# Kernel tuning notes

Hardware: AMD Instinct MI355X
Metric: run time of the kernel (lower is better)

The kernel has to match this reference:

```python
import jax, jax.numpy as jnp
import numpy as np

N = 120000   # current nodes
F = 256      # num_feat
H = 256      # num_hidden
L = 64       # num_logits
E_MP = 1000000  # message-passing edges
E = 200000      # scored edges
PREV = [60000, 80000, 100000]
PROX_WEIGHT = 0.3


def setup_inputs() -> dict:
    key = jax.random.key(0)
    ks = jax.random.split(key, 40)
    n = lambda k, shape, s=0.05: jax.random.normal(k, shape, dtype=jnp.float32) * s
    inp = {}
    inp["x"] = n(ks[0], (N, F), 1.0)
    inp["mp_adj"] = jax.random.randint(ks[1], (2, E_MP), 0, N)
    inp["edges"] = jax.random.randint(ks[2], (2, E), 0, N)
    inp["index"] = jax.random.randint(ks[3], (E,), 0, E)
    inp["prev_emb0"] = n(ks[4], (PREV[0], H), 1.0)
    inp["prev_emb1"] = n(ks[5], (PREV[1], H), 1.0)
    inp["prev_emb2"] = n(ks[6], (PREV[2], H), 1.0)
    # Module_L params
    inp["gc1_W"] = n(ks[7], (F, H))
    inp["gc1_b"] = jnp.zeros((H,), jnp.float32)
    inp["gc2_W"] = n(ks[8], (H, H))
    inp["gc2_b"] = jnp.zeros((H,), jnp.float32)
    inp["linear_W"] = n(ks[9], (2 * H, H))
    inp["linear_b"] = jnp.zeros((H,), jnp.float32)
    inp["weight_lin"] = n(ks[10], (H, H))
    inp["bias_lin"] = jnp.zeros((H,), jnp.float32)
    inp["w_q"] = n(ks[11], (H, H))
    inp["w_k"] = n(ks[12], (H, H))
    inp["w_v"] = n(ks[13], (H, H))
    # ensemble params
    inp["ml_w1"] = n(ks[14], (2 * H, H)); inp["ml_b1"] = jnp.zeros((H,), jnp.float32)
    inp["ml_w2"] = n(ks[15], (H, 1));     inp["ml_b2"] = jnp.zeros((1,), jnp.float32)
    inp["ms_w1"] = n(ks[16], (2 * H, H)); inp["ms_b1"] = jnp.zeros((H,), jnp.float32)
    inp["ms_w2"] = n(ks[17], (H, 1));     inp["ms_b2"] = jnp.zeros((1,), jnp.float32)
    inp["msdr_w"] = n(ks[18], (L, H));    inp["msdr_b"] = jnp.zeros((H,), jnp.float32)
    # Module_S logits and precomputed score tables
    inp["logits"] = n(ks[19], (N, L), 1.0)
    inp["ms_train_score"] = jax.random.uniform(ks[20], (E,), dtype=jnp.float32)
    inp["prox_train_score"] = jax.random.uniform(ks[21], (E,), dtype=jnp.float32)
    return inp


def _gcn(x, W, b, src, dst, n_nodes):
    xw = x @ W
    loop = jnp.arange(n_nodes)
    s = jnp.concatenate([src, loop])
    d = jnp.concatenate([dst, loop])
    deg = jax.ops.segment_sum(jnp.ones_like(d, dtype=xw.dtype), d, num_segments=n_nodes)
    dinv = jax.lax.rsqrt(jnp.maximum(deg, 1.0))
    norm = (dinv[s] * dinv[d])[:, None]
    out = jax.ops.segment_sum(xw[s] * norm, d, num_segments=n_nodes)
    return out + b


def _mean_max(a, b):
    return jnp.concatenate([(a + b) * 0.5, jnp.maximum(a, b)], axis=1)


def reference(x, mp_adj, edges, index, prev_emb0, prev_emb1, prev_emb2,
              gc1_W, gc1_b, gc2_W, gc2_b, linear_W, linear_b,
              weight_lin, bias_lin, w_q, w_k, w_v,
              ml_w1, ml_b1, ml_w2, ml_b2, ms_w1, ms_b1, ms_w2, ms_b2,
              msdr_w, msdr_b, logits, ms_train_score, prox_train_score):
    src_mp, dst_mp = mp_adj[0], mp_adj[1]
    # --- Module_L: 2-layer GCN encoder (dropout = identity in eval) ---
    h = jnp.tanh(_gcn(x, gc1_W, gc1_b, src_mp, dst_mp, N))
    emb = jnp.tanh(_gcn(h, gc2_W, gc2_b, src_mp, dst_mp, N))

    # --- ragged per-window temporal attention over previous snapshots ---
    prev = [prev_emb0, prev_emb1, prev_emb2]
    T = len(prev)
    start = 0
    parts = []
    for i in range(T):
        end = prev[i].shape[0]
        if end == N:
            break
        # stack snapshots i..T-1 plus current, restricted to window [start:end)
        stack = jnp.stack([prev[j][start:end] for j in range(i, T)] + [emb[start:end]], axis=0)  # [S,n,H]
        q = emb[start:end] @ w_q              # [n,H]
        k = stack @ w_k                        # [S,n,H]
        v = stack @ w_v                        # [S,n,H]
        attn = jnp.einsum('nh,snh->ns', q, k) / np.sqrt(np.float32(H))
        w = jax.nn.softmax(attn, axis=-1)      # [n,S]
        parts.append(jnp.einsum('ns,snh->nh', w, v))
        start = end
    if start != N:
        parts.append(emb[start:] @ w_v)
    attn_emb = jnp.concatenate(parts, axis=0)  # [N,H]

    emb2 = jnp.tanh(jnp.concatenate([emb, attn_emb], axis=1) @ linear_W + linear_b)  # [N,H]

    # --- symmetric bilinear edge scores ---
    sym = (weight_lin + weight_lin.T) * 0.5
    es, ed = edges[0], edges[1]
    sim = ((emb2[es] @ sym) * emb2[ed] + bias_lin).sum(axis=1)
    ml_scores = jax.nn.sigmoid(sim)            # [E]

    # --- Module_S / Proximity: table lookups ---
    ms_scores = ms_train_score[index]
    prox_scores = prox_train_score[index]

    # --- ensemble weighted sum ---
    scores = jnp.stack([ml_scores, ms_scores, prox_scores], axis=1)  # [E,3]
    ml_feat = _mean_max(emb2[es], emb2[ed])                          # [E,2H]
    a_ml = jnp.tanh(jnp.tanh(ml_feat @ ml_w1 + ml_b1) @ ml_w2 + ml_b2)
    r0 = jnp.tanh(logits[es] @ msdr_w + msdr_b)
    r1 = jnp.tanh(logits[ed] @ msdr_w + msdr_b)
    a_ms = jnp.tanh(jnp.tanh(_mean_max(r0, r1) @ ms_w1 + ms_b1) @ ms_w2 + ms_b2)
    a_px = jnp.full_like(a_ml, PROX_WEIGHT)
    attn_w = jax.nn.softmax(jnp.concatenate([a_ml, a_ms, a_px], axis=1), axis=1)  # [E,3]
    final = jnp.clip((scores * attn_w).sum(axis=1), 0.0, 1.0)
    return final
```

## Files before the change

kernel.cpp:

```cpp
#include <hip/hip_runtime.h>
#include <hip/hip_bf16.h>

#define Nn_   120000
#define F_    256
#define H_    256
#define L_    64
#define EMP_  1000000
#define E_    200000
#define P0_   60000
#define P1_   80000
#define P2_   100000
#define PROXW 0.3f

typedef __attribute__((ext_vector_type(8))) short bf16x8;
typedef __attribute__((ext_vector_type(4))) float f32x4;

__device__ inline float bf2f(unsigned short u) {
    union { unsigned int i; float f; } x; x.i = ((unsigned int)u) << 16; return x.f;
}
__device__ inline unsigned short f2bf(float f) {
    union { float f; unsigned int i; } x; x.f = f;
    unsigned int r = x.i + 0x7fffu + ((x.i >> 16) & 1u);
    return (unsigned short)(r >> 16);
}
__device__ inline float tanh_fast(float x) {
    float e = __expf(2.0f * x);
    return 1.0f - 2.0f * __builtin_amdgcn_rcpf(e + 1.0f);
}
__device__ inline float sigmoid_fast(float z) {
    return __builtin_amdgcn_rcpf(1.0f + __expf(-z));
}
__device__ inline int lds_off(int row, int s) {
    return row * 64 + ((s ^ ((row >> 1) & 3)) << 4);
}
__device__ inline void gload_lds16(const void* g, void* l) {
    __builtin_amdgcn_global_load_lds((const __attribute__((address_space(1))) void*)g,
                                     (__attribute__((address_space(3))) void*)l, 16, 0, 0);
}
__device__ inline void unpk8(uint4 u, float* o) {
    o[0] = bf2f(u.x & 0xffff); o[1] = bf2f(u.x >> 16);
    o[2] = bf2f(u.y & 0xffff); o[3] = bf2f(u.y >> 16);
    o[4] = bf2f(u.z & 0xffff); o[5] = bf2f(u.z >> 16);
    o[6] = bf2f(u.w & 0xffff); o[7] = bf2f(u.w >> 16);
}

__global__ void k_count(const int* __restrict__ dst, int* __restrict__ cnt, int n) {
    int e = blockIdx.x * 256 + threadIdx.x;
    if (e < n) atomicAdd(&cnt[dst[e]], 1);
}
__global__ void k_block_reduce(const int* __restrict__ cnt, int* __restrict__ bsum, int n) {
    __shared__ int s[256];
    int i = blockIdx.x * 256 + threadIdx.x;
    s[threadIdx.x] = (i < n) ? cnt[i] : 0;
    __syncthreads();
    for (int o = 128; o > 0; o >>= 1) {
        if (threadIdx.x < o) s[threadIdx.x] += s[threadIdx.x + o];
        __syncthreads();
    }
    if (threadIdx.x == 0) bsum[blockIdx.x] = s[0];
}
__global__ void k_scan_bsum(int* bsum, int nb) {
    if (threadIdx.x == 0 && blockIdx.x == 0) {
        int acc = 0;
        for (int i = 0; i < nb; i++) { int v = bsum[i]; bsum[i] = acc; acc += v; }
    }
}
__global__ void k_scan_final(const int* __restrict__ cnt, const int* __restrict__ bsum,
                             int* __restrict__ rowp, int n, int etot) {
    __shared__ int s[256];
    int tid = threadIdx.x;
    int i = blockIdx.x * 256 + tid;
    int v = (i < n) ? cnt[i] : 0;
    s[tid] = v;
    __syncthreads();
    for (int o = 1; o < 256; o <<= 1) {
        int t = 0;
        if (tid >= o) t = s[tid - o];
        __syncthreads();
        s[tid] += t;
        __syncthreads();
    }
    if (i < n) rowp[i] = bsum[blockIdx.x] + s[tid] - v;
    if (i == 0 && blockIdx.x == 0) rowp[n] = etot;
}
__global__ void k_fill(const int* __restrict__ src, const int* __restrict__ dst,
                       const int* __restrict__ rowp, int* __restrict__ fill,
                       int* __restrict__ csr, int n) {
    int e = blockIdx.x * 256 + threadIdx.x;
    if (e < n) {
        int d = dst[e];
        int p = atomicAdd(&fill[d], 1);
        csr[rowp[d] + p] = src[e];
    }
}
__global__ void k_dinv(const int* __restrict__ cnt, float* __restrict__ dinv, int n) {
    int i = blockIdx.x * 256 + threadIdx.x;
    if (i < n) dinv[i] = rsqrtf((float)cnt[i] + 1.0f);
}

#define TM 64
#define TN 64
#define TK 16
template <bool TRANSB>
__global__ void gemm_tiled(const float* __restrict__ A, const float* __restrict__ B,
                           float* __restrict__ C, int M, int K, int N) {
    __shared__ float As[TK][TM + 4];
    __shared__ float Bs[TK][TN + 4];
    int tid = threadIdx.x;
    int tx = tid & 15, ty = tid >> 4;
    int row0 = blockIdx.y * TM, col0 = blockIdx.x * TN;
    int lr = tid >> 2, lc4 = (tid & 3) * 4;
    float acc[4][4] = {};
    for (int k0 = 0; k0 < K; k0 += TK) {
        {
            int gr = row0 + lr;
            float4 v = make_float4(0.f, 0.f, 0.f, 0.f);
            if (gr < M) v = *(const float4*)(A + (size_t)gr * K + k0 + lc4);
            As[lc4 + 0][lr] = v.x; As[lc4 + 1][lr] = v.y;
            As[lc4 + 2][lr] = v.z; As[lc4 + 3][lr] = v.w;
        }
        {
            int n = tid & 63, kk0 = tid >> 6;
#pragma unroll
            for (int p = 0; p < 4; p++) {
                int kk = kk0 + p * 4;
                if (TRANSB) Bs[kk][n] = B[(size_t)(col0 + n) * K + k0 + kk];
                else        Bs[kk][n] = B[(size_t)(k0 + kk) * N + col0 + n];
            }
        }
        __syncthreads();
#pragma unroll
        for (int kk = 0; kk < TK; kk++) {
            float4 a = *(const float4*)&As[kk][ty * 4];
            float4 b = *(const float4*)&Bs[kk][tx * 4];
            float av[4] = {a.x, a.y, a.z, a.w};
            float bv[4] = {b.x, b.y, b.z, b.w};
#pragma unroll
            for (int i = 0; i < 4; i++)
#pragma unroll
                for (int j = 0; j < 4; j++) acc[i][j] += av[i] * bv[j];
        }
        __syncthreads();
    }
#pragma unroll
    for (int i = 0; i < 4; i++) {
        int r = row0 + ty * 4 + i;
        if (r >= M) continue;
#pragma unroll
        for (int j = 0; j < 4; j++) C[(size_t)r * N + col0 + tx * 4 + j] = acc[i][j];
    }
}

__global__ void k_cvt(const float* __restrict__ in, unsigned short* __restrict__ out, int n4) {
    int i = blockIdx.x * 256 + threadIdx.x;
    if (i >= n4) return;
    float4 v = ((const float4*)in)[i];
    ushort4 o;
    o.x = f2bf(v.x); o.y = f2bf(v.y); o.z = f2bf(v.z); o.w = f2bf(v.w);
    ((ushort4*)out)[i] = o;
}
__global__ void k_transpose_cvt(const float* __restrict__ W, unsigned short* __restrict__ Wt,
                                int R, int C) {
    int c = blockIdx.x;
    for (int r = threadIdx.x; r < R; r += 256)
        Wt[(size_t)c * R + r] = f2bf(W[(size_t)r * C + c]);
}
__global__ void k_sym_cvt(const float* __restrict__ W, unsigned short* __restrict__ symb) {
    int r = blockIdx.x, c = threadIdx.x;
    symb[r * 256 + c] = f2bf(0.5f * (W[r * 256 + c] + W[c * 256 + r]));
}
__global__ void k_bt512(const float* __restrict__ linW, const float* __restrict__ W2w,
                        unsigned short* __restrict__ Bt) {
    int idx = blockIdx.x * 256 + threadIdx.x;
    int n = idx >> 9, k = idx & 511;
    float v = (k < 256) ? linW[(size_t)k * 256 + n] : W2w[(size_t)(k - 256) * 256 + n];
    Bt[idx] = f2bf(v);
}
__global__ void k_sumb(const float* __restrict__ b, float* __restrict__ out) {
    __shared__ float s[256];
    int tid = threadIdx.x;
    s[tid] = b[tid];
    __syncthreads();
    for (int o = 128; o > 0; o >>= 1) {
        if (tid < o) s[tid] += s[tid + o];
        __syncthreads();
    }
    if (tid == 0) out[0] = s[0];
}
__global__ void k_packBF(const float* __restrict__ Wsrc, unsigned short* __restrict__ P) {
    int t = blockIdx.x * 256 + threadIdx.x;
    if (t >= 16384) return;
    int c = t >> 6, l = t & 63;
    int os = c >> 5, half = (c >> 4) & 1, colb = c & 15;
    int col = (colb << 4) + (l & 15);
    int k = (half << 8) + (os << 5) + ((l >> 4) << 3);
    bf16x8 v;
#pragma unroll
    for (int j = 0; j < 8; ++j) v[j] = (short)f2bf(Wsrc[(size_t)(k + j) * 256 + col]);
    *(bf16x8*)(P + (size_t)t * 8) = v;
}

__global__ __launch_bounds__(256)
void k_agg_bf(const unsigned short* __restrict__ xw, const int* __restrict__ rowp,
              const int* __restrict__ csr, const float* __restrict__ dinv,
              const float* __restrict__ bias, unsigned short* __restrict__ out) {
    int w = threadIdx.x >> 6, lane = threadIdx.x & 63;
    int v = blockIdx.x * 4 + w;
    if (v >= Nn_) return;
    const uint2* x64 = (const uint2*)xw;
    float a0 = 0.f, a1 = 0.f, a2 = 0.f, a3 = 0.f;
    int beg = rowp[v], end = rowp[v + 1];
    uint2 un = make_uint2(0, 0); float dn = 0.f;
    if (beg < end) {
        int s0 = csr[beg];
        dn = dinv[s0];
        un = x64[(size_t)s0 * 64 + lane];
    }
    for (int p = beg; p < end; ++p) {
        uint2 uc = un; float dc = dn;
        if (p + 1 < end) {
            int s1 = csr[p + 1];
            dn = dinv[s1];
            un = x64[(size_t)s1 * 64 + lane];
        }
        a0 += bf2f(uc.x & 0xffff) * dc;
        a1 += bf2f(uc.x >> 16) * dc;
        a2 += bf2f(uc.y & 0xffff) * dc;
        a3 += bf2f(uc.y >> 16) * dc;
    }
    float dv = dinv[v];
    uint2 us = x64[(size_t)v * 64 + lane];
    a0 = a0 * dv + bf2f(us.x & 0xffff) * dv * dv;
    a1 = a1 * dv + bf2f(us.x >> 16) * dv * dv;
    a2 = a2 * dv + bf2f(us.y & 0xffff) * dv * dv;
    a3 = a3 * dv + bf2f(us.y >> 16) * dv * dv;
    int c0 = lane * 4;
    float4 bv = *(const float4*)(bias + c0);
    uint2 ov;
    ov.x = (unsigned int)f2bf(tanh_fast(a0 + bv.x)) |
           ((unsigned int)f2bf(tanh_fast(a1 + bv.y)) << 16);
    ov.y = (unsigned int)f2bf(tanh_fast(a2 + bv.z)) |
           ((unsigned int)f2bf(tanh_fast(a3 + bv.w)) << 16);
    ((uint2*)out)[(size_t)v * 64 + lane] = ov;
}

template <bool BIAS, bool TANH>
__global__ __launch_bounds__(256)
void mfma_gemm(const unsigned short* __restrict__ A0, const unsigned short* __restrict__ A1,
               int Ksplit, int K, const unsigned short* __restrict__ Bt,
               const float* __restrict__ bias, unsigned short* __restrict__ Cb, int M) {
    __shared__ char lds[2][16384];
    int tid = threadIdx.x, lane = tid & 63, w = tid >> 6;
    int row0 = blockIdx.y * 128, col0 = blockIdx.x * 128;
    int wr = w >> 1, wc = w & 1;
    f32x4 acc[4][4] = {};
    int nk = K >> 5;

    auto stage = [&](int ks, int buf) {
        int k0 = ks << 5;
        #pragma unroll
        for (int j = 0; j < 4; ++j) {
            int ins = w + (j << 2);
            int lrow = ((ins & 7) << 4) + (lane >> 2);
            int p = lane & 3;
            int slog = p ^ ((lrow >> 1) & 3);
            char* ldst = lds[buf] + ((ins & 7) << 10) + ((ins >= 8) ? 8192 : 0);
            const unsigned short* src;
            if (ins < 8) {
                int grow = row0 + lrow;
                if (grow >= M) grow = M - 1;
                const unsigned short* Asrc; int kk, pitch;
                if (k0 < Ksplit) { Asrc = A0; kk = k0; pitch = Ksplit; }
                else             { Asrc = A1; kk = k0 - Ksplit; pitch = K - Ksplit; }
                src = Asrc + (size_t)grow * pitch + kk + (slog << 3);
            } else {
                int grow = col0 + lrow;
                src = Bt + (size_t)grow * K + k0 + (slog << 3);
            }
            gload_lds16(src, ldst);
        }
    };

    stage(0, 0);
    for (int ks = 0; ks < nk; ++ks) {
        int cur = ks & 1;
        if (ks + 1 < nk) {
            stage(ks + 1, cur ^ 1);
            asm volatile("s_waitcnt vmcnt(4)" ::: "memory");
        } else {
            asm volatile("s_waitcnt vmcnt(0)" ::: "memory");
        }
        __builtin_amdgcn_s_barrier();
        __builtin_amdgcn_sched_barrier(0);
        int s = lane >> 4, r16 = lane & 15;
        bf16x8 a[4], b[4];
        #pragma unroll
        for (int m = 0; m < 4; ++m) a[m] = *(const bf16x8*)(lds[cur] + lds_off(wr * 64 + m * 16 + r16, s));
        #pragma unroll
        for (int n = 0; n < 4; ++n) b[n] = *(const bf16x8*)(lds[cur] + 8192 + lds_off(wc * 64 + n * 16 + r16, s));
        __builtin_amdgcn_s_setprio(1);
        #pragma unroll
        for (int m = 0; m < 4; ++m)
            #pragma unroll
            for (int n = 0; n < 4; ++n)
                acc[m][n] = __builtin_amdgcn_mfma_f32_16x16x32_bf16(a[m], b[n], acc[m][n], 0, 0, 0);
        __builtin_amdgcn_s_setprio(0);
        __builtin_amdgcn_s_barrier();
        __builtin_amdgcn_sched_barrier(0);
    }
    int q = lane >> 4, r16 = lane & 15;
    float bv[4];
    #pragma unroll
    for (int n = 0; n < 4; ++n) bv[n] = BIAS ? bias[col0 + wc * 64 + n * 16 + r16] : 0.f;
    #pragma unroll
    for (int m = 0; m < 4; ++m) {
        #pragma unroll
        for (int i = 0; i < 4; ++i) {
            int row = row0 + wr * 64 + m * 16 + q * 4 + i;
            if (row >= M) continue;
            #pragma unroll
            for (int n = 0; n < 4; ++n) {
                int col = col0 + wc * 64 + n * 16 + r16;
                float v = acc[m][n][i];
                if (BIAS) v += bv[n];
                if (TANH) v = tanh_fast(v);
                Cb[(size_t)row * 256 + col] = f2bf(v);
            }
        }
    }
}

__global__ __launch_bounds__(256)
void k_attn_u2(const unsigned short* __restrict__ emb, const unsigned short* __restrict__ t,
               const float* __restrict__ p0, const float* __restrict__ p1,
               const float* __restrict__ p2, unsigned short* __restrict__ u) {
    int tid = threadIdx.x;
    int g = tid >> 4, l = tid & 15;
    int n = blockIdx.x * 16 + g;
    size_t eoff = (size_t)n * 256 + l * 16;
    const uint4* e16 = (const uint4*)(emb + eoff);
    uint4* u16 = (uint4*)(u + eoff);
    uint4 eb0 = e16[0], eb1 = e16[1];
    if (n >= P2_) { u16[0] = eb0; u16[1] = eb1; return; }
    float tv[16], ev[16];
    {
        const uint4* t16 = (const uint4*)(t + eoff);
        unpk8(t16[0], tv); unpk8(t16[1], tv + 8);
        unpk8(eb0, ev); unpk8(eb1, ev + 8);
    }
    float m = -3.0e38f, den = 0.f, o[16];
    #pragma unroll
    for (int i = 0; i < 16; i++) o[i] = 0.f;
    auto accum = [&](const float* sv) {
        float dt = 0.f;
        #pragma unroll
        for (int i = 0; i < 16; i++) dt += tv[i] * sv[i];
        dt += __shfl_xor(dt, 1);
        dt += __shfl_xor(dt, 2);
        dt += __shfl_xor(dt, 4);
        dt += __shfl_xor(dt, 8);
        float lg = dt * 0.0625f;
        float mn = fmaxf(m, lg);
        float s0 = __expf(m - mn), s1 = __expf(lg - mn);
        den = den * s0 + s1;
        #pragma unroll
        for (int i = 0; i < 16; i++) o[i] = o[i] * s0 + s1 * sv[i];
        m = mn;
    };
    auto accum_f32 = [&](const float* base) {
        float sv[16];
        const float4* b4 = (const float4*)(base + eoff);
        #pragma unroll
        for (int i = 0; i < 4; i++) {
            float4 q = b4[i];
            sv[4 * i] = q.x; sv[4 * i + 1] = q.y; sv[4 * i + 2] = q.z; sv[4 * i + 3] = q.w;
        }
        accum(sv);
    };
    if (n < P0_)      { accum_f32(p0); accum_f32(p1); accum_f32(p2); }
    else if (n < P1_) { accum_f32(p1); accum_f32(p2); }
    else              { accum_f32(p2); }
    accum(ev);
    float inv = __builtin_amdgcn_rcpf(den);
    unsigned short h[16];
    #pragma unroll
    for (int i = 0; i < 16; i++) h[i] = f2bf(o[i] * inv);
    uint4 r0, r1;
    r0.x = h[0] | ((unsigned int)h[1] << 16);  r0.y = h[2] | ((unsigned int)h[3] << 16);
    r0.z = h[4] | ((unsigned int)h[5] << 16);  r0.w = h[6] | ((unsigned int)h[7] << 16);
    r1.x = h[8] | ((unsigned int)h[9] << 16);  r1.y = h[10] | ((unsigned int)h[11] << 16);
    r1.z = h[12] | ((unsigned int)h[13] << 16); r1.w = h[14] | ((unsigned int)h[15] << 16);
    u16[0] = r0; u16[1] = r1;
}

template <bool SIM>
__global__ __launch_bounds__(256)
void mfma_edge3(const unsigned short* __restrict__ srcemb, const unsigned short* __restrict__ gsrc,
                const int* __restrict__ es, const int* __restrict__ ed,
                const unsigned short* __restrict__ PkF, const float* __restrict__ b1,
                const float* __restrict__ w2, const float* __restrict__ sumb,
                float* __restrict__ a_pre, float* __restrict__ mlsc) {
    __shared__ char lds[8192];
    __shared__ float red[64];
    int tid = threadIdx.x, lane = tid & 63, w = tid >> 6;
    int e0 = blockIdx.x * 64;
    int arow = tid >> 2, p = tid & 3;
    int ia = es[e0 + arow], ib = ed[e0 + arow];
    const unsigned short* ra = srcemb + (size_t)ia * 256;
    const unsigned short* rb = srcemb + (size_t)ib * 256;
    const unsigned short* rg = SIM ? (gsrc + (size_t)ia * 256) : nullptr;
    int slog = p ^ ((arow >> 1) & 3);
    int abase = arow * 64 + (p << 4);
    if (tid < 64) red[tid] = 0.f;
    float simacc = 0.f;
    f32x4 acc[4][4] = {};
    uint4 pa = *(const uint4*)(ra + (slog << 3));
    uint4 pb = *(const uint4*)(rb + (slog << 3));
    uint4 pg = make_uint4(0, 0, 0, 0);
    if (SIM) pg = *(const uint4*)(rg + (slog << 3));
    const bf16x8* BF = (const bf16x8*)PkF;
    for (int os = 0; os < 8; ++os) {
        {
            float fa[8], fb[8];
            unpk8(pa, fa); unpk8(pb, fb);
            bf16x8 vm, vx;
            #pragma unroll
            for (int i = 0; i < 8; i++) {
                vm[i] = (short)f2bf(0.5f * (fa[i] + fb[i]));
                vx[i] = (short)f2bf(fmaxf(fa[i], fb[i]));
            }
            *(bf16x8*)(lds + abase) = vm;
            *(bf16x8*)(lds + 4096 + abase) = vx;
            if (SIM) {
                float fg[8];
                unpk8(pg, fg);
                #pragma unroll
                for (int i = 0; i < 8; i++) simacc += fg[i] * fb[i];
            }
        }
        bf16x8 b0[4];
        #pragma unroll
        for (int n2 = 0; n2 < 4; ++n2)
            b0[n2] = BF[(((os << 1) << 4) + (w << 2) + n2) * 64 + lane];
        if (os < 7) {
            int cb = ((os + 1) << 5) + (slog << 3);
            pa = *(const uint4*)(ra + cb);
            pb = *(const uint4*)(rb + cb);
            if (SIM) pg = *(const uint4*)(rg + cb);
        }
        asm volatile("s_waitcnt lgkmcnt(0)" ::: "memory");
        __builtin_amdgcn_s_barrier();
        __builtin_amdgcn_sched_barrier(0);
        int s = lane >> 4, r16 = lane & 15;
        {
            bf16x8 a[4];
            #pragma unroll
            for (int m2 = 0; m2 < 4; ++m2)
                a[m2] = *(const bf16x8*)(lds + lds_off(m2 * 16 + r16, s));
            __builtin_amdgcn_s_setprio(1);
            #pragma unroll
            for (int m2 = 0; m2 < 4; ++m2)
                #pragma unroll
                for (int n2 = 0; n2 < 4; ++n2)
                    acc[m2][n2] = __builtin_amdgcn_mfma_f32_16x16x32_bf16(a[m2], b0[n2], acc[m2][n2], 0, 0, 0);
            __builtin_amdgcn_s_setprio(0);
        }
        {
            bf16x8 b1r[4], a[4];
            #pragma unroll
            for (int n2 = 0; n2 < 4; ++n2)
                b1r[n2] = BF[((((os << 1) + 1) << 4) + (w << 2) + n2) * 64 + lane];
            #pragma unroll
            for (int m2 = 0; m2 < 4; ++m2)
                a[m2] = *(const bf16x8*)(lds + 4096 + lds_off(m2 * 16 + r16, s));
            __builtin_amdgcn_s_setprio(1);
            #pragma unroll
            for (int m2 = 0; m2 < 4; ++m2)
                #pragma unroll
                for (int n2 = 0; n2 < 4; ++n2)
                    acc[m2][n2] = __builtin_amdgcn_mfma_f32_16x16x32_bf16(a[m2], b1r[n2], acc[m2][n2], 0, 0, 0);
            __builtin_amdgcn_s_setprio(0);
        }
        __builtin_amdgcn_s_barrier();
        __builtin_amdgcn_sched_barrier(0);
    }
    int q = lane >> 4, r16 = lane & 15;
    float b1c[4], w2c[4];
    #pragma unroll
    for (int n2 = 0; n2 < 4; ++n2) {
        int c = (w << 6) + n2 * 16 + r16;
        b1c[n2] = b1[c]; w2c[n2] = w2[c];
    }
    #pragma unroll
    for (int m2 = 0; m2 < 4; ++m2) {
        #pragma unroll
        for (int i = 0; i < 4; ++i) {
            int row = m2 * 16 + q * 4 + i;
            float ps = 0.f;
            #pragma unroll
            for (int n2 = 0; n2 < 4; ++n2) ps += tanh_fast(acc[m2][n2][i] + b1c[n2]) * w2c[n2];
            ps += __shfl_xor(ps, 1);
            ps += __shfl_xor(ps, 2);
            ps += __shfl_xor(ps, 4);
            ps += __shfl_xor(ps, 8);
            if (r16 == 0) atomicAdd(&red[row], ps);
        }
    }
    if (SIM) {
        simacc += __shfl_xor(simacc, 1);
        simacc += __shfl_xor(simacc, 2);
        if (p == 0) mlsc[e0 + arow] = sigmoid_fast(simacc + sumb[0]);
    }
    __syncthreads();
    if (tid < 64) a_pre[e0 + tid] = red[tid];
}

__global__ void k_final(const float* __restrict__ apml, const float* __restrict__ apms,
                        const float* __restrict__ mlsc, const float* __restrict__ mstr,
                        const float* __restrict__ pxtr, const int* __restrict__ index,
                        const float* __restrict__ mlb2, const float* __restrict__ msb2,
                        float* __restrict__ out) {
    int e = blockIdx.x * 256 + threadIdx.x;
    if (e >= E_) return;
    float aml = tanh_fast(apml[e] + mlb2[0]);
    float ams = tanh_fast(apms[e] + msb2[0]);
    float apx = PROXW;
    float m = fmaxf(aml, fmaxf(ams, apx));
    float wml = __expf(aml - m), wms = __expf(ams - m), wpx = __expf(apx - m);
    float inv = __builtin_amdgcn_rcpf(wml + wms + wpx);
    int idx = index[e];
    float v = (mlsc[e] * wml + mstr[idx] * wms + pxtr[idx] * wpx) * inv;
    out[e] = fminf(fmaxf(v, 0.f), 1.f);
}

__global__ void k_sentinel(float* out, int n) {
    int i = blockIdx.x * 256 + threadIdx.x;
    if (i < n) out[i] = -12345.0f;
}

extern "C" void kernel_launch(void* const* d_in, const int* in_sizes, int n_in,
                              void* d_out, int out_size, void* d_ws, size_t ws_size,
                              hipStream_t stream) {
    const float* x     = (const float*)d_in[0];
    const int*   mp    = (const int*)d_in[1];
    const int*   edges = (const int*)d_in[2];
    const int*   index = (const int*)d_in[3];
    const float* p0    = (const float*)d_in[4];
    const float* p1    = (const float*)d_in[5];
    const float* p2    = (const float*)d_in[6];
    const float* gc1W  = (const float*)d_in[7];
    const float* gc1b  = (const float*)d_in[8];
    const float* gc2W  = (const float*)d_in[9];
    const float* gc2b  = (const float*)d_in[10];
    const float* linW  = (const float*)d_in[11];
    const float* linb  = (const float*)d_in[12];
    const float* wlin  = (const float*)d_in[13];
    const float* blin  = (const float*)d_in[14];
    const float* wq    = (const float*)d_in[15];
    const float* wk    = (const float*)d_in[16];
    const float* wv    = (const float*)d_in[17];
    const float* mlw1  = (const float*)d_in[18];
    const float* mlb1  = (const float*)d_in[19];
    const float* mlw2  = (const float*)d_in[20];
    const float* mlb2  = (const float*)d_in[21];
    const float* msw1  = (const float*)d_in[22];
    const float* msb1  = (const float*)d_in[23];
    const float* msw2  = (const float*)d_in[24];
    const float* msb2  = (const float*)d_in[25];
    const float* msdrW = (const float*)d_in[26];
    const float* msdrb = (const float*)d_in[27];
    const float* logits = (const float*)d_in[28];
    const float* mstr  = (const float*)d_in[29];
    const float* pxtr  = (const float*)d_in[30];
    float* out = (float*)d_out;

    const int* src_mp = mp;
    const int* dst_mp = mp + EMP_;
    const int* es = edges;
    const int* ed = edges + E_;

    char* ws = (char*)d_ws;
    size_t off = 0;
    auto alloc = [&](size_t bytes) -> char* {
        off = (off + 255) & ~(size_t)255;
        char* r = ws + off;
        off += bytes;
        return r;
    };
    const size_t NODE_BF = (size_t)Nn_ * 256 * 2;
    unsigned short* W0 = (unsigned short*)alloc(NODE_BF);
    unsigned short* W1 = (unsigned short*)alloc(NODE_BF);
    unsigned short* W2 = (unsigned short*)alloc(NODE_BF);
    unsigned short* W3 = (unsigned short*)alloc(NODE_BF);
    unsigned short* W4 = (unsigned short*)alloc(NODE_BF);
    unsigned short* W5 = (unsigned short*)alloc(NODE_BF);
    int*   cnt  = (int*)alloc((size_t)Nn_ * 4);
    int*   rowp = (int*)alloc((size_t)(Nn_ + 1) * 4);
    int*   fill = (int*)alloc((size_t)Nn_ * 4);
    int*   csr  = (int*)alloc((size_t)EMP_ * 4);
    float* dinv = (float*)alloc((size_t)Nn_ * 4);
    int*   bsum = (int*)alloc(512 * 4);
    float* Mqk  = (float*)alloc(65536 * 4);
    float* W2wf = (float*)alloc(65536 * 4);
    unsigned short* gc1Wt = (unsigned short*)alloc(65536 * 2);
    unsigned short* gc2Wt = (unsigned short*)alloc(65536 * 2);
    unsigned short* MqkT  = (unsigned short*)alloc(65536 * 2);
    unsigned short* Bt512 = (unsigned short*)alloc(131072 * 2);
    unsigned short* symb  = (unsigned short*)alloc(65536 * 2);
    unsigned short* msdrWt = (unsigned short*)alloc(16384 * 2);
    unsigned short* mlPk  = (unsigned short*)alloc(131072 * 2);
    unsigned short* msPk  = (unsigned short*)alloc(131072 * 2);
    float* apml = (float*)alloc((size_t)E_ * 4);
    float* apms = (float*)alloc((size_t)E_ * 4);
    float* mlsc = (float*)alloc((size_t)E_ * 4);
    float* sumb = (float*)alloc(256);

    if (off > ws_size) {
        k_sentinel<<<(E_ + 255) / 256, 256, 0, stream>>>(out, E_);
        return;
    }

    hipMemsetAsync(cnt, 0, (size_t)Nn_ * 4, stream);
    hipMemsetAsync(fill, 0, (size_t)Nn_ * 4, stream);

    const int NB = (Nn_ + 255) / 256;
    const int EB = (EMP_ + 255) / 256;

    k_cvt<<<30000, 256, 0, stream>>>(x, W0, Nn_ * 256 / 4);
    k_transpose_cvt<<<256, 256, 0, stream>>>(gc1W, gc1Wt, 256, 256);
    k_transpose_cvt<<<256, 256, 0, stream>>>(gc2W, gc2Wt, 256, 256);
    k_transpose_cvt<<<256, 256, 0, stream>>>(msdrW, msdrWt, 64, 256);
    k_packBF<<<64, 256, 0, stream>>>(mlw1, mlPk);
    k_packBF<<<64, 256, 0, stream>>>(msw1, msPk);
    k_sym_cvt<<<256, 256, 0, stream>>>(wlin, symb);
    k_sumb<<<1, 256, 0, stream>>>(blin, sumb);
    dim3 gSmall(4, 4);
    gemm_tiled<true><<<gSmall, 256, 0, stream>>>(wq, wk, Mqk, 256, 256, 256);
    gemm_tiled<false><<<gSmall, 256, 0, stream>>>(wv, linW + 256 * 256, W2wf, 256, 256, 256);
    k_transpose_cvt<<<256, 256, 0, stream>>>(Mqk, MqkT, 256, 256);
    k_bt512<<<512, 256, 0, stream>>>(linW, W2wf, Bt512);

    k_count<<<EB, 256, 0, stream>>>(dst_mp, cnt, EMP_);
    k_block_reduce<<<NB, 256, 0, stream>>>(cnt, bsum, Nn_);
    k_scan_bsum<<<1, 64, 0, stream>>>(bsum, NB);
    k_scan_final<<<NB, 256, 0, stream>>>(cnt, bsum, rowp, Nn_, EMP_);
    k_fill<<<EB, 256, 0, stream>>>(src_mp, dst_mp, rowp, fill, csr, EMP_);
    k_dinv<<<NB, 256, 0, stream>>>(cnt, dinv, Nn_);

    dim3 gFull(2, (Nn_ + 127) / 128);
    dim3 gT(2, (P2_ + 127) / 128);
    const int AGG_B = (Nn_ + 3) / 4;

    mfma_gemm<false, false><<<gFull, 256, 0, stream>>>(W0, W0, 256, 256, gc1Wt, nullptr, W1, Nn_);
    k_agg_bf<<<AGG_B, 256, 0, stream>>>(W1, rowp, csr, dinv, gc1b, W2);
    mfma_gemm<false, false><<<gFull, 256, 0, stream>>>(W2, W2, 256, 256, gc2Wt, nullptr, W1, Nn_);
    k_agg_bf<<<AGG_B, 256, 0, stream>>>(W1, rowp, csr, dinv, gc2b, W3);

    mfma_gemm<false, false><<<gT, 256, 0, stream>>>(W3, W3, 256, 256, MqkT, nullptr, W4, P2_);
    k_attn_u2<<<Nn_ / 16, 256, 0, stream>>>(W3, W4, p0, p1, p2, W4);

    mfma_gemm<true, true><<<gFull, 256, 0, stream>>>(W3, W4, 256, 512, Bt512, linb, W5, Nn_);

    mfma_gemm<false, false><<<gFull, 256, 0, stream>>>(W5, W5, 256, 256, symb, nullptr, W0, Nn_);

    k_cvt<<<7500, 256, 0, stream>>>(logits, W1, Nn_ * 64 / 4);
    mfma_gemm<true, true><<<gFull, 256, 0, stream>>>(W1, W1, 64, 64, msdrWt, msdrb, W2, Nn_);

    mfma_edge3<true><<<E_ / 64, 256, 0, stream>>>(W5, W0, es, ed, mlPk, mlb1, mlw2, sumb, apml, mlsc);
    mfma_edge3<false><<<E_ / 64, 256, 0, stream>>>(W2, nullptr, es, ed, msPk, msb1, msw2, sumb, apms, nullptr);

    k_final<<<(E_ + 255) / 256, 256, 0, stream>>>(apml, apms, mlsc, mstr, pxtr, index, mlb2, msb2, out);
}
```

Measured before the change: 1.010 ms.

## Merge weight-prep kernels and deepen gather prefetch in edge MLP kernel

Nine small weight-preparation launches are folded into two multi-role kernels, which removes launch overhead and serialization between tiny grids. The edge MLP kernel now prefetches four row chunks ahead in registers instead of one, so gather latency on the random embedding rows is better hidden. It also computes mean and max directly on packed bf16 words rather than unpacking to float arrays. The deeper prefetch raises register pressure, and loading the weight fragments after the barrier could expose their latency.

```diff
diff --git a/kernel.cpp b/kernel.cpp
--- a/kernel.cpp
+++ b/kernel.cpp
@@ -42,6 +42,24 @@
     o[2] = bf2f(u.y & 0xffff); o[3] = bf2f(u.y >> 16);
     o[4] = bf2f(u.z & 0xffff); o[5] = bf2f(u.z >> 16);
     o[6] = bf2f(u.w & 0xffff); o[7] = bf2f(u.w >> 16);
+}
+__device__ inline void meanmax_u(unsigned int ua, unsigned int ub,
+                                 unsigned int& um, unsigned int& ux) {
+    float alo = __uint_as_float(ua << 16);
+    float ahi = __uint_as_float(ua & 0xffff0000u);
+    float blo = __uint_as_float(ub << 16);
+    float bhi = __uint_as_float(ub & 0xffff0000u);
+    um = (unsigned int)f2bf((alo + blo) * 0.5f) |
+         ((unsigned int)f2bf((ahi + bhi) * 0.5f) << 16);
+    ux = (__float_as_uint(fmaxf(alo, blo)) >> 16) |
+         (__float_as_uint(fmaxf(ahi, bhi)) & 0xffff0000u);
+}
+__device__ inline float dot2_u(unsigned int ug, unsigned int ub) {
+    float gl = __uint_as_float(ug << 16);
+    float gh = __uint_as_float(ug & 0xffff0000u);
+    float bl = __uint_as_float(ub << 16);
+    float bh = __uint_as_float(ub & 0xffff0000u);
+    return fmaf(gl, bl, gh * bh);
 }
 
 __global__ void k_count(const int* __restrict__ dst, int* __restrict__ cnt, int n) {
@@ -159,37 +177,10 @@
     o.x = f2bf(v.x); o.y = f2bf(v.y); o.z = f2bf(v.z); o.w = f2bf(v.w);
     ((ushort4*)out)[i] = o;
 }
-__global__ void k_transpose_cvt(const float* __restrict__ W, unsigned short* __restrict__ Wt,
-                                int R, int C) {
-    int c = blockIdx.x;
-    for (int r = threadIdx.x; r < R; r += 256)
-        Wt[(size_t)c * R + r] = f2bf(W[(size_t)r * C + c]);
-}
-__global__ void k_sym_cvt(const float* __restrict__ W, unsigned short* __restrict__ symb) {
-    int r = blockIdx.x, c = threadIdx.x;
-    symb[r * 256 + c] = f2bf(0.5f * (W[r * 256 + c] + W[c * 256 + r]));
-}
-__global__ void k_bt512(const float* __restrict__ linW, const float* __restrict__ W2w,
-                        unsigned short* __restrict__ Bt) {
-    int idx = blockIdx.x * 256 + threadIdx.x;
-    int n = idx >> 9, k = idx & 511;
-    float v = (k < 256) ? linW[(size_t)k * 256 + n] : W2w[(size_t)(k - 256) * 256 + n];
-    Bt[idx] = f2bf(v);
-}
-__global__ void k_sumb(const float* __restrict__ b, float* __restrict__ out) {
-    __shared__ float s[256];
-    int tid = threadIdx.x;
-    s[tid] = b[tid];
-    __syncthreads();
-    for (int o = 128; o > 0; o >>= 1) {
-        if (tid < o) s[tid] += s[tid + o];
-        __syncthreads();
-    }
-    if (tid == 0) out[0] = s[0];
-}
-__global__ void k_packBF(const float* __restrict__ Wsrc, unsigned short* __restrict__ P) {
-    int t = blockIdx.x * 256 + threadIdx.x;
-    if (t >= 16384) return;
+
+__device__ inline void packBF_task(const float* __restrict__ Wsrc,
+                                   unsigned short* __restrict__ P, int blk) {
+    int t = blk * 256 + threadIdx.x;
     int c = t >> 6, l = t & 63;
     int os = c >> 5, half = (c >> 4) & 1, colb = c & 15;
     int col = (colb << 4) + (l & 15);
@@ -198,6 +189,57 @@
 #pragma unroll
     for (int j = 0; j < 8; ++j) v[j] = (short)f2bf(Wsrc[(size_t)(k + j) * 256 + col]);
     *(bf16x8*)(P + (size_t)t * 8) = v;
+}
+
+__global__ void k_prep1(const float* __restrict__ gc1W, const float* __restrict__ gc2W,
+                        const float* __restrict__ msdrW, const float* __restrict__ wlin,
+                        const float* __restrict__ blin, const float* __restrict__ mlw1,
+                        const float* __restrict__ msw1,
+                        unsigned short* __restrict__ gc1Wt, unsigned short* __restrict__ gc2Wt,
+                        unsigned short* __restrict__ msdrWt, unsigned short* __restrict__ symb,
+                        float* __restrict__ sumb, unsigned short* __restrict__ mlPk,
+                        unsigned short* __restrict__ msPk) {
+    __shared__ float s[256];
+    int b = blockIdx.x, tid = threadIdx.x;
+    if (b < 256) {
+        int c = b;
+        for (int r = tid; r < 256; r += 256) gc1Wt[c * 256 + r] = f2bf(gc1W[(size_t)r * 256 + c]);
+    } else if (b < 512) {
+        int c = b - 256;
+        for (int r = tid; r < 256; r += 256) gc2Wt[c * 256 + r] = f2bf(gc2W[(size_t)r * 256 + c]);
+    } else if (b < 768) {
+        int c = b - 512;
+        if (tid < 64) msdrWt[c * 64 + tid] = f2bf(msdrW[(size_t)tid * 256 + c]);
+    } else if (b < 1024) {
+        int r = b - 768, c = tid;
+        symb[r * 256 + c] = f2bf(0.5f * (wlin[r * 256 + c] + wlin[c * 256 + r]));
+    } else if (b == 1024) {
+        s[tid] = blin[tid];
+        __syncthreads();
+        for (int o = 128; o > 0; o >>= 1) {
+            if (tid < o) s[tid] += s[tid + o];
+            __syncthreads();
+        }
+        if (tid == 0) sumb[0] = s[0];
+    } else if (b < 1089) {
+        packBF_task(mlw1, mlPk, b - 1025);
+    } else {
+        packBF_task(msw1, msPk, b - 1089);
+    }
+}
+__global__ void k_prep2(const float* __restrict__ Mqk, const float* __restrict__ linW,
+                        const float* __restrict__ W2w, unsigned short* __restrict__ MqkT,
+                        unsigned short* __restrict__ Bt) {
+    int b = blockIdx.x, tid = threadIdx.x;
+    if (b < 256) {
+        int c = b;
+        for (int r = tid; r < 256; r += 256) MqkT[c * 256 + r] = f2bf(Mqk[(size_t)r * 256 + c]);
+    } else {
+        int idx = (b - 256) * 256 + tid;
+        int n = idx >> 9, k = idx & 511;
+        float v = (k < 256) ? linW[(size_t)k * 256 + n] : W2w[(size_t)(k - 256) * 256 + n];
+        Bt[idx] = f2bf(v);
+    }
 }
 
 __global__ __launch_bounds__(256)
@@ -395,7 +437,7 @@
 
 template <bool SIM>
 __global__ __launch_bounds__(256)
-void mfma_edge3(const unsigned short* __restrict__ srcemb, const unsigned short* __restrict__ gsrc,
+void mfma_edge4(const unsigned short* __restrict__ srcemb, const unsigned short* __restrict__ gsrc,
                 const int* __restrict__ es, const int* __restrict__ ed,
                 const unsigned short* __restrict__ PkF, const float* __restrict__ b1,
                 const float* __restrict__ w2, const float* __restrict__ sumb,
@@ -410,50 +452,60 @@
     const unsigned short* rb = srcemb + (size_t)ib * 256;
     const unsigned short* rg = SIM ? (gsrc + (size_t)ia * 256) : nullptr;
     int slog = p ^ ((arow >> 1) & 3);
+    int co = slog << 3;
     int abase = arow * 64 + (p << 4);
     if (tid < 64) red[tid] = 0.f;
+    f32x4 acc[4][4] = {};
     float simacc = 0.f;
-    f32x4 acc[4][4] = {};
-    uint4 pa = *(const uint4*)(ra + (slog << 3));
-    uint4 pb = *(const uint4*)(rb + (slog << 3));
-    uint4 pg = make_uint4(0, 0, 0, 0);
-    if (SIM) pg = *(const uint4*)(rg + (slog << 3));
     const bf16x8* BF = (const bf16x8*)PkF;
+    uint4 pa0 = *(const uint4*)(ra + co);
+    uint4 pb0 = *(const uint4*)(rb + co);
+    uint4 pa1 = *(const uint4*)(ra + 32 + co);
+    uint4 pb1 = *(const uint4*)(rb + 32 + co);
+    uint4 pa2 = *(const uint4*)(ra + 64 + co);
+    uint4 pb2 = *(const uint4*)(rb + 64 + co);
+    uint4 pa3 = *(const uint4*)(ra + 96 + co);
+    uint4 pb3 = *(const uint4*)(rb + 96 + co);
+    uint4 pg0 = make_uint4(0, 0, 0, 0), pg1 = pg0, pg2 = pg0, pg3 = pg0;
+    if (SIM) {
+        pg0 = *(const uint4*)(rg + co);
+        pg1 = *(const uint4*)(rg + 32 + co);
+        pg2 = *(const uint4*)(rg + 64 + co);
+        pg3 = *(const uint4*)(rg + 96 + co);
+    }
+    #pragma unroll
     for (int os = 0; os < 8; ++os) {
+        uint4 ua = pa0, ub = pb0, ug = pg0;
+        pa0 = pa1; pa1 = pa2; pa2 = pa3;
+        pb0 = pb1; pb1 = pb2; pb2 = pb3;
+        if (SIM) { pg0 = pg1; pg1 = pg2; pg2 = pg3; }
+        if (os < 4) {
+            int cb = ((os + 4) << 5) + co;
+            pa3 = *(const uint4*)(ra + cb);
+            pb3 = *(const uint4*)(rb + cb);
+            if (SIM) pg3 = *(const uint4*)(rg + cb);
+        }
         {
-            float fa[8], fb[8];
-            unpk8(pa, fa); unpk8(pb, fb);
-            bf16x8 vm, vx;
-            #pragma unroll
-            for (int i = 0; i < 8; i++) {
-                vm[i] = (short)f2bf(0.5f * (fa[i] + fb[i]));
-                vx[i] = (short)f2bf(fmaxf(fa[i], fb[i]));
-            }
-            *(bf16x8*)(lds + abase) = vm;
-            *(bf16x8*)(lds + 4096 + abase) = vx;
-            if (SIM) {
-                float fg[8];
-                unpk8(pg, fg);
-                #pragma unroll
-                for (int i = 0; i < 8; i++) simacc += fg[i] * fb[i];
-            }
-        }
-        bf16x8 b0[4];
-        #pragma unroll
-        for (int n2 = 0; n2 < 4; ++n2)
-            b0[n2] = BF[(((os << 1) << 4) + (w << 2) + n2) * 64 + lane];
-        if (os < 7) {
-            int cb = ((os + 1) << 5) + (slog << 3);
-            pa = *(const uint4*)(ra + cb);
-            pb = *(const uint4*)(rb + cb);
-            if (SIM) pg = *(const uint4*)(rg + cb);
+            unsigned int m0, x0, m1, x1, m2, x2, m3, x3;
+            meanmax_u(ua.x, ub.x, m0, x0);
+            meanmax_u(ua.y, ub.y, m1, x1);
+            meanmax_u(ua.z, ub.z, m2, x2);
+            meanmax_u(ua.w, ub.w, m3, x3);
+            *(uint4*)(lds + abase) = make_uint4(m0, m1, m2, m3);
+            *(uint4*)(lds + 4096 + abase) = make_uint4(x0, x1, x2, x3);
+            if (SIM)
+                simacc += dot2_u(ug.x, ub.x) + dot2_u(ug.y, ub.y) +
+                          dot2_u(ug.z, ub.z) + dot2_u(ug.w, ub.w);
         }
         asm volatile("s_waitcnt lgkmcnt(0)" ::: "memory");
         __builtin_amdgcn_s_barrier();
         __builtin_amdgcn_sched_barrier(0);
         int s = lane >> 4, r16 = lane & 15;
         {
-            bf16x8 a[4];
+            bf16x8 b0[4], a[4];
+            #pragma unroll
+            for (int n2 = 0; n2 < 4; ++n2)
+                b0[n2] = BF[(size_t)((((os << 1) << 4) + (w << 2) + n2) * 64 + lane)];
             #pragma unroll
             for (int m2 = 0; m2 < 4; ++m2)
                 a[m2] = *(const bf16x8*)(lds + lds_off(m2 * 16 + r16, s));
@@ -469,7 +521,7 @@
             bf16x8 b1r[4], a[4];
             #pragma unroll
             for (int n2 = 0; n2 < 4; ++n2)
-                b1r[n2] = BF[((((os << 1) + 1) << 4) + (w << 2) + n2) * 64 + lane];
+                b1r[n2] = BF[(size_t)(((((os << 1) + 1) << 4) + (w << 2) + n2) * 64 + lane)];
             #pragma unroll
             for (int m2 = 0; m2 < 4; ++m2)
                 a[m2] = *(const bf16x8*)(lds + 4096 + lds_off(m2 * 16 + r16, s));
@@ -627,18 +679,12 @@
     const int EB = (EMP_ + 255) / 256;
 
     k_cvt<<<30000, 256, 0, stream>>>(x, W0, Nn_ * 256 / 4);
-    k_transpose_cvt<<<256, 256, 0, stream>>>(gc1W, gc1Wt, 256, 256);
-    k_transpose_cvt<<<256, 256, 0, stream>>>(gc2W, gc2Wt, 256, 256);
-    k_transpose_cvt<<<256, 256, 0, stream>>>(msdrW, msdrWt, 64, 256);
-    k_packBF<<<64, 256, 0, stream>>>(mlw1, mlPk);
-    k_packBF<<<64, 256, 0, stream>>>(msw1, msPk);
-    k_sym_cvt<<<256, 256, 0, stream>>>(wlin, symb);
-    k_sumb<<<1, 256, 0, stream>>>(blin, sumb);
+    k_prep1<<<1153, 256, 0, stream>>>(gc1W, gc2W, msdrW, wlin, blin, mlw1, msw1,
+                                      gc1Wt, gc2Wt, msdrWt, symb, sumb, mlPk, msPk);
     dim3 gSmall(4, 4);
     gemm_tiled<true><<<gSmall, 256, 0, stream>>>(wq, wk, Mqk, 256, 256, 256);
     gemm_tiled<false><<<gSmall, 256, 0, stream>>>(wv, linW + 256 * 256, W2wf, 256, 256, 256);
-    k_transpose_cvt<<<256, 256, 0, stream>>>(Mqk, MqkT, 256, 256);
-    k_bt512<<<512, 256, 0, stream>>>(linW, W2wf, Bt512);
+    k_prep2<<<768, 256, 0, stream>>>(Mqk, linW, W2wf, MqkT, Bt512);
 
     k_count<<<EB, 256, 0, stream>>>(dst_mp, cnt, EMP_);
     k_block_reduce<<<NB, 256, 0, stream>>>(cnt, bsum, Nn_);
@@ -666,8 +712,8 @@
     k_cvt<<<7500, 256, 0, stream>>>(logits, W1, Nn_ * 64 / 4);
     mfma_gemm<true, true><<<gFull, 256, 0, stream>>>(W1, W1, 64, 64, msdrWt, msdrb, W2, Nn_);
 
-    mfma_edge3<true><<<E_ / 64, 256, 0, stream>>>(W5, W0, es, ed, mlPk, mlb1, mlw2, sumb, apml, mlsc);
-    mfma_edge3<false><<<E_ / 64, 256, 0, stream>>>(W2, nullptr, es, ed, msPk, msb1, msw2, sumb, apms, nullptr);
+    mfma_edge4<true><<<E_ / 64, 256, 0, stream>>>(W5, W0, es, ed, mlPk, mlb1, mlw2, sumb, apml, mlsc);
+    mfma_edge4<false><<<E_ / 64, 256, 0, stream>>>(W2, nullptr, es, ed, msPk, msb1, msw2, sumb, apms, nullptr);
 
     k_final<<<(E_ + 255) / 256, 256, 0, stream>>>(apml, apms, mlsc, mstr, pxtr, index, mlb2, msb2, out);
 }
```

Result: no change. 1.028 ms (+1.8%).
